# Performance work log

Hardware: AMD Instinct MI355X
Metric: run time of the kernel (lower is better)

The kernel has to match this reference:

```python
import jax, jax.numpy as jnp
import numpy as np

SCALE = 1.0 / np.sqrt(128.0)  # 1/sqrt(head_dim)


def setup_inputs() -> dict:
    key = jax.random.key(0)
    kq, kk, kv, km = jax.random.split(key, 4)
    B, N, T, S, H = 2, 32, 2048, 2048, 128
    q = jax.random.normal(kq, (B, N, T, H), dtype=jnp.float32)
    k = jax.random.normal(kk, (B, N, S, H), dtype=jnp.float32)
    v = jax.random.normal(kv, (B, N, S, H), dtype=jnp.float32)
    mask = jax.random.randint(km, (B, 1, T, S), 0, 2).astype(jnp.bool_)
    return {"q": q, "k": k, "v": v, "mask": mask}


def reference(q, k, v, mask):
    # [b,n,t,s] attention logits
    attn_logits = jnp.einsum('bnth,bnsh->bnts', q, k) * SCALE
    mask_value = jnp.finfo(attn_logits.dtype).min
    attn_logits = jnp.where(mask, attn_logits, mask_value)
    attn_weights = jax.nn.softmax(attn_logits, axis=-1)
    # [b,n,t,s] @ [b,n,s,h] -> [b,n,t,h]
    return jnp.matmul(attn_weights, v)
```

## Files before the change

kernel.cpp:

```cpp
#include <hip/hip_runtime.h>
#include <hip/hip_bf16.h>

typedef unsigned short u16;
typedef unsigned int u32;
typedef unsigned long long u64;
typedef short bf16x8 __attribute__((ext_vector_type(8)));
typedef float f32x4 __attribute__((ext_vector_type(4)));

#define T_DIM 2048
#define S_DIM 2048
#define H_DIM 128
#define KT 32
#define NKT (S_DIM / KT)
#define P_STR 40
#define SCL 0.12753257480082588f
#define NEG_BIG -1e30f

#define KB_OFF 0u
#define KB_BYTES (64u * 2048u * 128u * 2u)
#define VT_OFF KB_BYTES
#define VT_BYTES (64u * 2048u * 128u * 2u)
#define BM_OFF (KB_BYTES + VT_BYTES)
#define BM_BYTES (2u * 2048u * 2048u / 8u)
#define WS_NEED ((size_t)(BM_OFF + BM_BYTES))

static __device__ __forceinline__ u16 f2b(float x) {
  return __builtin_bit_cast(u16, __float2bfloat16(x));
}
static __device__ __forceinline__ bf16x8 cvt8(float4 a, float4 b) {
  bf16x8 f;
  f[0] = (short)f2b(a.x); f[1] = (short)f2b(a.y);
  f[2] = (short)f2b(a.z); f[3] = (short)f2b(a.w);
  f[4] = (short)f2b(b.x); f[5] = (short)f2b(b.y);
  f[6] = (short)f2b(b.z); f[7] = (short)f2b(b.w);
  return f;
}

template<int CTRL>
static __device__ __forceinline__ float dppf(float x) {
  return __builtin_bit_cast(float,
    __builtin_amdgcn_update_dpp(0, __builtin_bit_cast(int, x), CTRL, 0xf, 0xf, true));
}
static __device__ __forceinline__ float red16_sum(float x) {
  x += dppf<0xB1>(x);
  x += dppf<0x4E>(x);
  x += dppf<0x141>(x);
  x += dppf<0x140>(x);
  return x;
}
static __device__ __forceinline__ float red16_max(float x) {
  x = fmaxf(x, dppf<0xB1>(x));
  x = fmaxf(x, dppf<0x4E>(x));
  x = fmaxf(x, dppf<0x141>(x));
  x = fmaxf(x, dppf<0x140>(x));
  return x;
}

static __device__ __forceinline__ void gl_lds16(const void* g, void* l) {
  __builtin_amdgcn_global_load_lds(
      (const __attribute__((address_space(1))) void*)g,
      (__attribute__((address_space(3))) void*)l, 16, 0, 0);
}

__global__ __launch_bounds__(256)
void cvt_k(const float* __restrict__ src, u16* __restrict__ dst) {
  size_t g = (size_t)(blockIdx.x * 256 + threadIdx.x) * 8;
  float4 a = *(const float4*)(src + g);
  float4 b = *(const float4*)(src + g + 4);
  *(bf16x8*)(dst + g) = cvt8(a, b);
}

__global__ __launch_bounds__(256)
void vt_pack(const float* __restrict__ V, u16* __restrict__ Vt) {
  __shared__ u16 Lt[32][136];
  const int hd = blockIdx.x >> 6;
  const int t  = blockIdx.x & 63;
  const int tid = threadIdx.x;
  const float* src = V + ((size_t)hd * S_DIM + (size_t)t * 32) * H_DIM;
  {
    int r = tid >> 3, h0 = (tid & 7) * 16;
    const float* sp = src + (size_t)r * H_DIM + h0;
    float4 a0 = *(const float4*)sp,      a1 = *(const float4*)(sp + 4);
    float4 a2 = *(const float4*)(sp + 8), a3 = *(const float4*)(sp + 12);
    *(bf16x8*)&Lt[r][h0]     = cvt8(a0, a1);
    *(bf16x8*)&Lt[r][h0 + 8] = cvt8(a2, a3);
  }
  __syncthreads();
  {
    int h = tid >> 1, k0 = (tid & 1) * 16;
    bf16x8 o0, o1;
#pragma unroll
    for (int j = 0; j < 8; ++j) o0[j] = (short)Lt[k0 + j][h];
#pragma unroll
    for (int j = 0; j < 8; ++j) o1[j] = (short)Lt[k0 + 8 + j][h];
    u16* dp = Vt + ((size_t)hd * 64 + t) * 4096 + (size_t)tid * 16;
    *(bf16x8*)dp = o0;
    *(bf16x8*)(dp + 8) = o1;
  }
}

__global__ __launch_bounds__(256)
void pack_mask(const int* __restrict__ M, u64* __restrict__ BM) {
  const int row  = blockIdx.x * 4 + (threadIdx.x >> 6);
  const int lane = threadIdx.x & 63;
  const int* mr = M + (size_t)row * S_DIM;
  u64* br = BM + (size_t)row * (S_DIM / 64);
  for (int s0 = 0; s0 < S_DIM; s0 += 64) {
    u64 b = __ballot(mr[s0 + lane] != 0);
    if (lane == 0) br[s0 >> 6] = b;
  }
}

__global__ __launch_bounds__(256, 2)
void attn_fwd(const float* __restrict__ Q, const u16* __restrict__ Kb,
              const u16* __restrict__ Vtb, const u32* __restrict__ BM,
              float* __restrict__ O)
{
  __shared__ __align__(16) u16 KT2[2][32 * 128];
  __shared__ __align__(16) u16 VT2[2][128 * 32];
  __shared__ __align__(16) u16 Pt[4][32 * P_STR];

  const int tid  = threadIdx.x;
  const int wave = tid >> 6;
  const int lane = tid & 63;
  const int col  = lane & 15;
  const int quad = lane >> 4;

  const int head   = blockIdx.x >> 4;
  const int qblock = blockIdx.x & 15;
  const int batch  = head >> 5;
  const int q0w    = qblock * 128 + wave * 32;

  const float* Qh   = Q + (size_t)head * T_DIM * H_DIM;
  const char*  kb_t = (const char*)(Kb  + (size_t)head * S_DIM * H_DIM);
  const char*  vt_t = (const char*)(Vtb + (size_t)head * S_DIM * H_DIM);
  const u32*   bmr  = BM + ((size_t)batch * T_DIM + q0w) * (S_DIM / 32);

  int koffb[2], voffb[2], lbase[2];
#pragma unroll
  for (int i = 0; i < 2; ++i) {
    int slot = wave * 64 + lane + 256 * i;
    int kr = slot >> 4, kc = slot & 15;
    koffb[i] = kr * 256 + ((kc ^ (kr & 15)) << 4);
    int vh = slot >> 2, vc = slot & 3;
    voffb[i] = vh * 64 + (((vc ^ vh) & 3) << 4);
    lbase[i] = (wave * 64 + 256 * i) * 8;
  }

  bf16x8 qf[2][4];
#pragma unroll
  for (int mi = 0; mi < 2; ++mi) {
    const float* qp = Qh + (size_t)(q0w + mi * 16 + col) * H_DIM + quad * 8;
#pragma unroll
    for (int s = 0; s < 4; ++s) {
      float4 a = *(const float4*)(qp + 32 * s);
      float4 b = *(const float4*)(qp + 32 * s + 4);
      a.x *= SCL; a.y *= SCL; a.z *= SCL; a.w *= SCL;
      b.x *= SCL; b.y *= SCL; b.z *= SCL; b.w *= SCL;
      qf[mi][s] = cvt8(a, b);
    }
  }

  f32x4 o[2][8];
#pragma unroll
  for (int mi = 0; mi < 2; ++mi)
#pragma unroll
    for (int c = 0; c < 8; ++c) o[mi][c] = (f32x4){0.f, 0.f, 0.f, 0.f};
  float l_p[2][4] = {{0.f,0.f,0.f,0.f},{0.f,0.f,0.f,0.f}};

  u16* Pw = &Pt[wave][0];

#pragma unroll
  for (int i = 0; i < 2; ++i) {
    gl_lds16(kb_t + koffb[i], (void*)&KT2[0][lbase[i]]);
    gl_lds16(vt_t + voffb[i], (void*)&VT2[0][lbase[i]]);
  }

  for (int kt = 0; kt < NKT; ++kt) {
    asm volatile("s_waitcnt vmcnt(0) lgkmcnt(0)\n\ts_barrier" ::: "memory");

    if (kt + 1 < NKT) {
      const char* ks = kb_t + (size_t)(kt + 1) * 8192;
      const char* vs = vt_t + (size_t)(kt + 1) * 8192;
      const int nb = (kt + 1) & 1;
#pragma unroll
      for (int i = 0; i < 2; ++i) {
        gl_lds16(ks + koffb[i], (void*)&KT2[nb][lbase[i]]);
        gl_lds16(vs + voffb[i], (void*)&VT2[nb][lbase[i]]);
      }
    }

    const u16* Kc = &KT2[kt & 1][0];
    const u16* Vc = &VT2[kt & 1][0];

    f32x4 sc00 = {0,0,0,0}, sc01 = {0,0,0,0}, sc10 = {0,0,0,0}, sc11 = {0,0,0,0};
#pragma unroll
    for (int s = 0; s < 4; ++s) {
      const int g = s * 4 + quad;
      bf16x8 kf0 = *(const bf16x8*)&Kc[col * 128 + ((g ^ col) & 15) * 8];
      bf16x8 kf1 = *(const bf16x8*)&Kc[(col + 16) * 128 + ((g ^ col) & 15) * 8];
      sc00 = __builtin_amdgcn_mfma_f32_16x16x32_bf16(qf[0][s], kf0, sc00, 0, 0, 0);
      sc01 = __builtin_amdgcn_mfma_f32_16x16x32_bf16(qf[0][s], kf1, sc01, 0, 0, 0);
      sc10 = __builtin_amdgcn_mfma_f32_16x16x32_bf16(qf[1][s], kf0, sc10, 0, 0, 0);
      sc11 = __builtin_amdgcn_mfma_f32_16x16x32_bf16(qf[1][s], kf1, sc11, 0, 0, 0);
    }

#pragma unroll
    for (int mi = 0; mi < 2; ++mi) {
      f32x4 s0 = mi ? sc10 : sc00;
      f32x4 s1 = mi ? sc11 : sc01;
#pragma unroll
      for (int i = 0; i < 4; ++i) {
        const int r = mi * 16 + quad * 4 + i;
        u32 w = bmr[(size_t)r * (S_DIM / 32) + kt];
        float p0 = ((w >> col) & 1u)        ? exp2f(s0[i]) : 0.f;
        float p1 = ((w >> (col + 16)) & 1u) ? exp2f(s1[i]) : 0.f;
        l_p[mi][i] += p0 + p1;
        Pw[r * P_STR + col]      = f2b(p0);
        Pw[r * P_STR + col + 16] = f2b(p1);
      }
    }

    bf16x8 pf0 = *(const bf16x8*)&Pw[col * P_STR + quad * 8];
    bf16x8 pf1 = *(const bf16x8*)&Pw[(col + 16) * P_STR + quad * 8];
#pragma unroll
    for (int c = 0; c < 8; ++c) {
      bf16x8 vf = *(const bf16x8*)&Vc[(c * 16 + col) * 32 + ((quad ^ col) & 3) * 8];
      o[0][c] = __builtin_amdgcn_mfma_f32_16x16x32_bf16(pf0, vf, o[0][c], 0, 0, 0);
      o[1][c] = __builtin_amdgcn_mfma_f32_16x16x32_bf16(pf1, vf, o[1][c], 0, 0, 0);
    }
  }

  float* Oh = O + (size_t)head * T_DIM * H_DIM;
#pragma unroll
  for (int mi = 0; mi < 2; ++mi)
#pragma unroll
    for (int i = 0; i < 4; ++i) {
      float inv = 1.0f / red16_sum(l_p[mi][i]);
      float* orow = Oh + (size_t)(q0w + mi * 16 + quad * 4 + i) * H_DIM;
#pragma unroll
      for (int c = 0; c < 8; ++c)
        orow[c * 16 + col] = o[mi][c][i] * inv;
    }
}

__global__ __launch_bounds__(256, 2)
void attn_fb(const float* __restrict__ Q, const float* __restrict__ K,
             const float* __restrict__ V, const int* __restrict__ M,
             float* __restrict__ O)
{
  __shared__ __align__(16) u16 Kt[32 * 136];
  __shared__ __align__(16) u16 Vt[H_DIM * 40];
  __shared__ __align__(16) u16 Pt[4][32 * P_STR];

  const int tid  = threadIdx.x;
  const int wave = tid >> 6;
  const int lane = tid & 63;
  const int col  = lane & 15;
  const int quad = lane >> 4;
  const int head   = blockIdx.x >> 4;
  const int qblock = blockIdx.x & 15;
  const int batch  = head >> 5;
  const int q0w    = qblock * 128 + wave * 32;

  const float* Qh = Q + (size_t)head * T_DIM * H_DIM;
  const float* Kp = K + (size_t)head * S_DIM * H_DIM;
  const float* Vp = V + (size_t)head * S_DIM * H_DIM;
  const int*   Mb = M + (size_t)batch * T_DIM * S_DIM + (size_t)q0w * S_DIM;

  const int krow = tid >> 4;
  const int kc8  = (tid & 15) * 8;
  const float* kp0 = Kp + (size_t)krow * H_DIM + kc8;
  const float* kp1 = kp0 + (size_t)16 * H_DIM;
  const int vrow = tid & 31;
  const int vc8  = (tid >> 5) * 8;
  const float* vp0 = Vp + (size_t)vrow * H_DIM + vc8;
  const float* vp1 = vp0 + 64;

  bf16x8 qf[2][4];
#pragma unroll
  for (int mi = 0; mi < 2; ++mi) {
    const float* qp = Qh + (size_t)(q0w + mi * 16 + col) * H_DIM + quad * 8;
#pragma unroll
    for (int s = 0; s < 4; ++s) {
      float4 a = *(const float4*)(qp + 32 * s);
      float4 b = *(const float4*)(qp + 32 * s + 4);
      a.x *= SCL; a.y *= SCL; a.z *= SCL; a.w *= SCL;
      b.x *= SCL; b.y *= SCL; b.z *= SCL; b.w *= SCL;
      qf[mi][s] = cvt8(a, b);
    }
  }

  f32x4 o[2][8];
#pragma unroll
  for (int mi = 0; mi < 2; ++mi)
#pragma unroll
    for (int c = 0; c < 8; ++c) o[mi][c] = (f32x4){0.f,0.f,0.f,0.f};
  float l_p[2][4] = {{0.f,0.f,0.f,0.f},{0.f,0.f,0.f,0.f}};

  float4 ka00 = *(const float4*)kp0, ka01 = *(const float4*)(kp0 + 4);
  float4 ka10 = *(const float4*)kp1, ka11 = *(const float4*)(kp1 + 4);
  float4 va00 = *(const float4*)vp0, va01 = *(const float4*)(vp0 + 4);
  float4 va10 = *(const float4*)vp1, va11 = *(const float4*)(vp1 + 4);

  u16* Pw = &Pt[wave][0];

  for (int kt = 0; kt < NKT; ++kt) {
    asm volatile("s_waitcnt lgkmcnt(0)\n\ts_barrier" ::: "memory");
    *(bf16x8*)&Kt[krow * 136 + kc8]        = cvt8(ka00, ka01);
    *(bf16x8*)&Kt[(krow + 16) * 136 + kc8] = cvt8(ka10, ka11);
    {
      u16* v0 = &Vt[vc8 * 40 + vrow];
      v0[0*40] = f2b(va00.x); v0[1*40] = f2b(va00.y);
      v0[2*40] = f2b(va00.z); v0[3*40] = f2b(va00.w);
      v0[4*40] = f2b(va01.x); v0[5*40] = f2b(va01.y);
      v0[6*40] = f2b(va01.z); v0[7*40] = f2b(va01.w);
      u16* v1 = &Vt[(vc8 + 64) * 40 + vrow];
      v1[0*40] = f2b(va10.x); v1[1*40] = f2b(va10.y);
      v1[2*40] = f2b(va10.z); v1[3*40] = f2b(va10.w);
      v1[4*40] = f2b(va11.x); v1[5*40] = f2b(va11.y);
      v1[6*40] = f2b(va11.z); v1[7*40] = f2b(va11.w);
    }
    if (kt + 1 < NKT) {
      kp0 += KT * H_DIM; kp1 += KT * H_DIM; vp0 += KT * H_DIM; vp1 += KT * H_DIM;
      ka00 = *(const float4*)kp0; ka01 = *(const float4*)(kp0 + 4);
      ka10 = *(const float4*)kp1; ka11 = *(const float4*)(kp1 + 4);
      va00 = *(const float4*)vp0; va01 = *(const float4*)(vp0 + 4);
      va10 = *(const float4*)vp1; va11 = *(const float4*)(vp1 + 4);
    }
    asm volatile("s_waitcnt lgkmcnt(0)\n\ts_barrier" ::: "memory");

    f32x4 sc00 = {0,0,0,0}, sc01 = {0,0,0,0}, sc10 = {0,0,0,0}, sc11 = {0,0,0,0};
#pragma unroll
    for (int s = 0; s < 4; ++s) {
      bf16x8 kf0 = *(const bf16x8*)&Kt[col * 136 + s * 32 + quad * 8];
      bf16x8 kf1 = *(const bf16x8*)&Kt[(col + 16) * 136 + s * 32 + quad * 8];
      sc00 = __builtin_amdgcn_mfma_f32_16x16x32_bf16(qf[0][s], kf0, sc00, 0, 0, 0);
      sc01 = __builtin_amdgcn_mfma_f32_16x16x32_bf16(qf[0][s], kf1, sc01, 0, 0, 0);
      sc10 = __builtin_amdgcn_mfma_f32_16x16x32_bf16(qf[1][s], kf0, sc10, 0, 0, 0);
      sc11 = __builtin_amdgcn_mfma_f32_16x16x32_bf16(qf[1][s], kf1, sc11, 0, 0, 0);
    }

#pragma unroll
    for (int mi = 0; mi < 2; ++mi) {
      f32x4 s0 = mi ? sc10 : sc00;
      f32x4 s1 = mi ? sc11 : sc01;
#pragma unroll
      for (int i = 0; i < 4; ++i) {
        const int r = mi * 16 + quad * 4 + i;
        const int* mrow = Mb + (size_t)r * S_DIM + kt * KT;
        float p0 = mrow[col]      ? exp2f(s0[i]) : 0.f;
        float p1 = mrow[col + 16] ? exp2f(s1[i]) : 0.f;
        l_p[mi][i] += p0 + p1;
        Pw[r * P_STR + col]      = f2b(p0);
        Pw[r * P_STR + col + 16] = f2b(p1);
      }
    }

    bf16x8 pf0 = *(const bf16x8*)&Pw[col * P_STR + quad * 8];
    bf16x8 pf1 = *(const bf16x8*)&Pw[(col + 16) * P_STR + quad * 8];
#pragma unroll
    for (int c = 0; c < 8; ++c) {
      bf16x8 vf = *(const bf16x8*)&Vt[(c * 16 + col) * 40 + quad * 8];
      o[0][c] = __builtin_amdgcn_mfma_f32_16x16x32_bf16(pf0, vf, o[0][c], 0, 0, 0);
      o[1][c] = __builtin_amdgcn_mfma_f32_16x16x32_bf16(pf1, vf, o[1][c], 0, 0, 0);
    }
  }

  float* Oh = O + (size_t)head * T_DIM * H_DIM;
#pragma unroll
  for (int mi = 0; mi < 2; ++mi)
#pragma unroll
    for (int i = 0; i < 4; ++i) {
      float inv = 1.0f / red16_sum(l_p[mi][i]);
      float* orow = Oh + (size_t)(q0w + mi * 16 + quad * 4 + i) * H_DIM;
#pragma unroll
      for (int c = 0; c < 8; ++c)
        orow[c * 16 + col] = o[mi][c][i] * inv;
    }
}

extern "C" void kernel_launch(void* const* d_in, const int* in_sizes, int n_in,
                              void* d_out, int out_size, void* d_ws, size_t ws_size,
                              hipStream_t stream) {
  const float* q = (const float*)d_in[0];
  const float* k = (const float*)d_in[1];
  const float* v = (const float*)d_in[2];
  const int*   m = (const int*)d_in[3];
  float* out = (float*)d_out;

  if (d_ws != nullptr && ws_size >= WS_NEED) {
    u16* kb  = (u16*)((char*)d_ws + KB_OFF);
    u16* vtb = (u16*)((char*)d_ws + VT_OFF);
    u64* bm  = (u64*)((char*)d_ws + BM_OFF);
    cvt_k<<<dim3(8192), dim3(256), 0, stream>>>(k, kb);
    vt_pack<<<dim3(4096), dim3(256), 0, stream>>>(v, vtb);
    pack_mask<<<dim3((2 * T_DIM) / 4), dim3(256), 0, stream>>>(m, bm);
    attn_fwd<<<dim3(1024), dim3(256), 0, stream>>>(q, kb, vtb, (const u32*)bm, out);
  } else {
    attn_fb<<<dim3(1024), dim3(256), 0, stream>>>(q, k, v, m, out);
  }
}
```

Before: 492.5 us.

## Keep softmax P in registers via transposed QK MFMA and permlane swaps

Computes S^T by swapping the MFMA operands so each lane holds probabilities for one query row. The probabilities are packed to bf16 with v_cvt_pk_bf16_f32 and rearranged into the PV A-operand layout with permlane16/32 swaps, which removes the per-wave LDS round trip for P. The mask words are prefetched one tile ahead, and the row-sum reduction is moved to the end through LDS. Launch bounds are raised to 4 waves per SIMD and the block index is swizzled so blocks sharing a head are spread differently, which risks register spills.

```diff
diff --git a/kernel.cpp b/kernel.cpp
--- a/kernel.cpp
+++ b/kernel.cpp
@@ -6,6 +6,7 @@
 typedef unsigned long long u64;
 typedef short bf16x8 __attribute__((ext_vector_type(8)));
 typedef float f32x4 __attribute__((ext_vector_type(4)));
+typedef u32 u32x4 __attribute__((ext_vector_type(4)));
 
 #define T_DIM 2048
 #define S_DIM 2048
@@ -36,6 +37,18 @@
   return f;
 }
 
+static __device__ __forceinline__ u32 cvtpk_bf16(float lo, float hi) {
+  u32 r;
+  asm("v_cvt_pk_bf16_f32 %0, %1, %2" : "=v"(r) : "v"(lo), "v"(hi));
+  return r;
+}
+static __device__ __forceinline__ void pl32_swap(u32& a, u32& b) {
+  asm("v_permlane32_swap_b32 %0, %1" : "+v"(a), "+v"(b));
+}
+static __device__ __forceinline__ void pl16_swap(u32& a, u32& b) {
+  asm("v_permlane16_swap_b32 %0, %1" : "+v"(a), "+v"(b));
+}
+
 template<int CTRL>
 static __device__ __forceinline__ float dppf(float x) {
   return __builtin_bit_cast(float,
@@ -46,13 +59,6 @@
   x += dppf<0x4E>(x);
   x += dppf<0x141>(x);
   x += dppf<0x140>(x);
-  return x;
-}
-static __device__ __forceinline__ float red16_max(float x) {
-  x = fmaxf(x, dppf<0xB1>(x));
-  x = fmaxf(x, dppf<0x4E>(x));
-  x = fmaxf(x, dppf<0x141>(x));
-  x = fmaxf(x, dppf<0x140>(x));
   return x;
 }
 
@@ -111,14 +117,13 @@
   }
 }
 
-__global__ __launch_bounds__(256, 2)
+__global__ __launch_bounds__(256, 4)
 void attn_fwd(const float* __restrict__ Q, const u16* __restrict__ Kb,
               const u16* __restrict__ Vtb, const u32* __restrict__ BM,
               float* __restrict__ O)
 {
   __shared__ __align__(16) u16 KT2[2][32 * 128];
   __shared__ __align__(16) u16 VT2[2][128 * 32];
-  __shared__ __align__(16) u16 Pt[4][32 * P_STR];
 
   const int tid  = threadIdx.x;
   const int wave = tid >> 6;
@@ -126,15 +131,17 @@
   const int col  = lane & 15;
   const int quad = lane >> 4;
 
-  const int head   = blockIdx.x >> 4;
-  const int qblock = blockIdx.x & 15;
+  const int wg = ((blockIdx.x & 7) << 7) | (blockIdx.x >> 3);
+  const int head   = wg >> 4;
+  const int qblock = wg & 15;
   const int batch  = head >> 5;
   const int q0w    = qblock * 128 + wave * 32;
 
   const float* Qh   = Q + (size_t)head * T_DIM * H_DIM;
   const char*  kb_t = (const char*)(Kb  + (size_t)head * S_DIM * H_DIM);
   const char*  vt_t = (const char*)(Vtb + (size_t)head * S_DIM * H_DIM);
-  const u32*   bmr  = BM + ((size_t)batch * T_DIM + q0w) * (S_DIM / 32);
+  const u32*   bmr0 = BM + ((size_t)batch * T_DIM + q0w + col) * (S_DIM / 32);
+  const u32*   bmr1 = bmr0 + (size_t)16 * (S_DIM / 32);
 
   int koffb[2], voffb[2], lbase[2];
 #pragma unroll
@@ -166,15 +173,14 @@
   for (int mi = 0; mi < 2; ++mi)
 #pragma unroll
     for (int c = 0; c < 8; ++c) o[mi][c] = (f32x4){0.f, 0.f, 0.f, 0.f};
-  float l_p[2][4] = {{0.f,0.f,0.f,0.f},{0.f,0.f,0.f,0.f}};
-
-  u16* Pw = &Pt[wave][0];
+  float l_p[2] = {0.f, 0.f};
 
 #pragma unroll
   for (int i = 0; i < 2; ++i) {
     gl_lds16(kb_t + koffb[i], (void*)&KT2[0][lbase[i]]);
     gl_lds16(vt_t + voffb[i], (void*)&VT2[0][lbase[i]]);
   }
+  u32 wm0 = bmr0[0], wm1 = bmr1[0];
 
   for (int kt = 0; kt < NKT; ++kt) {
     asm volatile("s_waitcnt vmcnt(0) lgkmcnt(0)\n\ts_barrier" ::: "memory");
@@ -193,55 +199,79 @@
     const u16* Kc = &KT2[kt & 1][0];
     const u16* Vc = &VT2[kt & 1][0];
 
-    f32x4 sc00 = {0,0,0,0}, sc01 = {0,0,0,0}, sc10 = {0,0,0,0}, sc11 = {0,0,0,0};
+    u32 w0 = wm0, w1 = wm1;
+    if (kt + 1 < NKT) { wm0 = bmr0[kt + 1]; wm1 = bmr1[kt + 1]; }
+
+    f32x4 s00 = {0,0,0,0}, s10 = {0,0,0,0}, s01 = {0,0,0,0}, s11 = {0,0,0,0};
 #pragma unroll
     for (int s = 0; s < 4; ++s) {
       const int g = s * 4 + quad;
       bf16x8 kf0 = *(const bf16x8*)&Kc[col * 128 + ((g ^ col) & 15) * 8];
       bf16x8 kf1 = *(const bf16x8*)&Kc[(col + 16) * 128 + ((g ^ col) & 15) * 8];
-      sc00 = __builtin_amdgcn_mfma_f32_16x16x32_bf16(qf[0][s], kf0, sc00, 0, 0, 0);
-      sc01 = __builtin_amdgcn_mfma_f32_16x16x32_bf16(qf[0][s], kf1, sc01, 0, 0, 0);
-      sc10 = __builtin_amdgcn_mfma_f32_16x16x32_bf16(qf[1][s], kf0, sc10, 0, 0, 0);
-      sc11 = __builtin_amdgcn_mfma_f32_16x16x32_bf16(qf[1][s], kf1, sc11, 0, 0, 0);
-    }
-
+      s00 = __builtin_amdgcn_mfma_f32_16x16x32_bf16(kf0, qf[0][s], s00, 0, 0, 0);
+      s10 = __builtin_amdgcn_mfma_f32_16x16x32_bf16(kf1, qf[0][s], s10, 0, 0, 0);
+      s01 = __builtin_amdgcn_mfma_f32_16x16x32_bf16(kf0, qf[1][s], s01, 0, 0, 0);
+      s11 = __builtin_amdgcn_mfma_f32_16x16x32_bf16(kf1, qf[1][s], s11, 0, 0, 0);
+    }
+
+    bf16x8 pA[2];
 #pragma unroll
     for (int mi = 0; mi < 2; ++mi) {
-      f32x4 s0 = mi ? sc10 : sc00;
-      f32x4 s1 = mi ? sc11 : sc01;
+      f32x4 x0 = mi ? s01 : s00;
+      f32x4 x1 = mi ? s11 : s10;
+      u32 w = (mi ? w1 : w0) >> (quad * 4);
+      float p0[4], p1[4];
 #pragma unroll
       for (int i = 0; i < 4; ++i) {
-        const int r = mi * 16 + quad * 4 + i;
-        u32 w = bmr[(size_t)r * (S_DIM / 32) + kt];
-        float p0 = ((w >> col) & 1u)        ? exp2f(s0[i]) : 0.f;
-        float p1 = ((w >> (col + 16)) & 1u) ? exp2f(s1[i]) : 0.f;
-        l_p[mi][i] += p0 + p1;
-        Pw[r * P_STR + col]      = f2b(p0);
-        Pw[r * P_STR + col + 16] = f2b(p1);
+        p0[i] = ((w >> i) & 1u)        ? exp2f(x0[i]) : 0.f;
+        p1[i] = ((w >> (16 + i)) & 1u) ? exp2f(x1[i]) : 0.f;
       }
-    }
-
-    bf16x8 pf0 = *(const bf16x8*)&Pw[col * P_STR + quad * 8];
-    bf16x8 pf1 = *(const bf16x8*)&Pw[(col + 16) * P_STR + quad * 8];
+      l_p[mi] += ((p0[0] + p0[1]) + (p0[2] + p0[3])) +
+                 ((p1[0] + p1[1]) + (p1[2] + p1[3]));
+      u32 fa = cvtpk_bf16(p0[0], p0[1]);
+      u32 fb = cvtpk_bf16(p0[2], p0[3]);
+      u32 fc = cvtpk_bf16(p1[0], p1[1]);
+      u32 fd = cvtpk_bf16(p1[2], p1[3]);
+      pl32_swap(fa, fc); pl16_swap(fa, fc);
+      pl32_swap(fb, fd); pl16_swap(fb, fd);
+      u32x4 fr = {fa, fb, fc, fd};
+      pA[mi] = __builtin_bit_cast(bf16x8, fr);
+    }
+
 #pragma unroll
     for (int c = 0; c < 8; ++c) {
       bf16x8 vf = *(const bf16x8*)&Vc[(c * 16 + col) * 32 + ((quad ^ col) & 3) * 8];
-      o[0][c] = __builtin_amdgcn_mfma_f32_16x16x32_bf16(pf0, vf, o[0][c], 0, 0, 0);
-      o[1][c] = __builtin_amdgcn_mfma_f32_16x16x32_bf16(pf1, vf, o[1][c], 0, 0, 0);
-    }
-  }
+      o[0][c] = __builtin_amdgcn_mfma_f32_16x16x32_bf16(pA[0], vf, o[0][c], 0, 0, 0);
+      o[1][c] = __builtin_amdgcn_mfma_f32_16x16x32_bf16(pA[1], vf, o[1][c], 0, 0, 0);
+    }
+  }
+
+  float* sred = (float*)(&KT2[0][0]) + wave * 32;
+#pragma unroll
+  for (int mi = 0; mi < 2; ++mi) {
+    u32 a = __builtin_bit_cast(u32, l_p[mi]), b = a;
+    pl32_swap(a, b);
+    float s2 = __builtin_bit_cast(float, a) + __builtin_bit_cast(float, b);
+    u32 c = __builtin_bit_cast(u32, s2), d = c;
+    pl16_swap(c, d);
+    float tot = __builtin_bit_cast(float, c) + __builtin_bit_cast(float, d);
+    if (quad == 0) sred[mi * 16 + col] = tot;
+  }
+  asm volatile("s_waitcnt lgkmcnt(0)" ::: "memory");
 
   float* Oh = O + (size_t)head * T_DIM * H_DIM;
 #pragma unroll
-  for (int mi = 0; mi < 2; ++mi)
+  for (int mi = 0; mi < 2; ++mi) {
+    float4 lv = *(const float4*)&sred[mi * 16 + quad * 4];
+    float invs[4] = {1.0f / lv.x, 1.0f / lv.y, 1.0f / lv.z, 1.0f / lv.w};
 #pragma unroll
     for (int i = 0; i < 4; ++i) {
-      float inv = 1.0f / red16_sum(l_p[mi][i]);
       float* orow = Oh + (size_t)(q0w + mi * 16 + quad * 4 + i) * H_DIM;
 #pragma unroll
       for (int c = 0; c < 8; ++c)
-        orow[c * 16 + col] = o[mi][c][i] * inv;
-    }
+        orow[c * 16 + col] = o[mi][c][i] * invs[i];
+    }
+  }
 }
 
 __global__ __launch_bounds__(256, 2)
```

New measurement: 566.9 us. 1.15x slower.
